# Kernel tuning notes

Hardware: AMD Instinct MI355X
Metric: run time of the kernel (lower is better)

The kernel has to match this reference:

```python
import jax, jax.numpy as jnp
import numpy as np

VOCAB = 100000
DIM = 300
N, P, D = 4096, 10, 17  # samples, paths per sample (2C), padded path depth


def setup_inputs() -> dict:
    key = jax.random.key(0)
    k1, k2, k3, k4, k5 = jax.random.split(key, 5)
    word_idx = jax.random.randint(k1, (N,), 0, VOCAB)
    paths = jax.random.randint(k2, (N, P, D), 0, VOCAB - 1)   # inner-node ids
    labels = jax.random.randint(k3, (N, P, D), 0, 2)          # branch directions
    emb1 = jax.random.normal(k4, (VOCAB, DIM), dtype=jnp.float32) * 0.1
    emb2 = jax.random.normal(k5, (VOCAB - 1, DIM), dtype=jnp.float32) * 0.1
    return {"word_idx": word_idx, "paths": paths, "labels": labels,
            "emb1": emb1, "emb2": emb2}


def reference(word_idx, paths, labels, emb1, emb2):
    # proj = embedding_1(x_idx): [N, DIM]
    proj = emb1[word_idx]
    # hierarchy_vectors = embedding_2(dir_path): [N, P, D, DIM]
    hvecs = emb2[paths]
    # output = sigmoid(proj @ hvecs.T), batched over (N, P): [N, P, D]
    logits = jnp.einsum('nd,npkd->npk', proj, hvecs)
    output = jax.nn.sigmoid(logits)
    # mask[output >= 0.5] = 1; target[mask == label] = 1
    mask = (output >= 0.5).astype(labels.dtype)
    target = (mask == labels).astype(jnp.float32)
    return output, target
```

## Files before the change

kernel.cpp:

```cpp
#include <hip/hip_runtime.h>
#include <math.h>

#define NN 4096
#define PP 10
#define DD 17
#define DIM 300
#define NPD (NN * PP * DD)

__global__ __launch_bounds__(256) void hs_fwd_kernel(
    const int* __restrict__ word_idx,
    const int* __restrict__ paths,
    const int* __restrict__ labels,
    const float* __restrict__ emb1,
    const float* __restrict__ emb2,
    float* __restrict__ out,
    float* __restrict__ target)
{
    const int wave = (int)((blockIdx.x * blockDim.x + threadIdx.x) >> 6);
    const int lane = (int)(threadIdx.x & 63);
    if (wave >= NN * PP) return;
    const int n = wave / PP;

    const float* e1 = emb1 + (long long)word_idx[n] * DIM;
    const float pr0 = e1[lane];
    const float pr1 = e1[lane + 64];
    const float pr2 = e1[lane + 128];
    const float pr3 = e1[lane + 192];
    const float pr4 = (lane < DIM - 256) ? e1[lane + 256] : 0.0f;

    const long long base = (long long)wave * DD;
    const int my_path  = (lane < DD) ? paths[base + lane]  : 0;
    const int my_label = (lane < DD) ? labels[base + lane] : 0;

    float my_logit = 0.0f;
    #pragma unroll
    for (int k = 0; k < DD; ++k) {
        const int row = __shfl(my_path, k);
        const float* e2 = emb2 + (long long)row * DIM;
        float acc = pr0 * e2[lane]
                  + pr1 * e2[lane + 64]
                  + pr2 * e2[lane + 128]
                  + pr3 * e2[lane + 192];
        if (lane < DIM - 256) acc += pr4 * e2[lane + 256];
        #pragma unroll
        for (int off = 32; off > 0; off >>= 1)
            acc += __shfl_xor(acc, off);
        if (lane == k) my_logit = acc;
    }

    if (lane < DD) {
        const float o = 1.0f / (1.0f + expf(-my_logit));
        out[base + lane] = o;
        const int mask = (o >= 0.5f) ? 1 : 0;
        target[base + lane] = (mask == my_label) ? 1.0f : 0.0f;
    }
}

extern "C" void kernel_launch(void* const* d_in, const int* in_sizes, int n_in,
                              void* d_out, int out_size, void* d_ws, size_t ws_size,
                              hipStream_t stream) {
    const int*   word_idx = (const int*)d_in[0];
    const int*   paths    = (const int*)d_in[1];
    const int*   labels   = (const int*)d_in[2];
    const float* emb1     = (const float*)d_in[3];
    const float* emb2     = (const float*)d_in[4];

    float* out    = (float*)d_out;
    float* target = (float*)d_out + NPD;

    const int total_waves = NN * PP;
    const int waves_per_block = 4;
    const int blocks = (total_waves + waves_per_block - 1) / waves_per_block;

    hs_fwd_kernel<<<blocks, 256, 0, stream>>>(word_idx, paths, labels, emb1, emb2, out, target);
}
```

Baseline: 324.1 us.

## Vectorize embedding loads as float4 and process two path rows per wave

Embedding rows are now read as float4, and each wave splits into two 32-lane halves, each handling a different path node at once. This cuts the number of load instructions and the loop iterations (9 instead of 17) and shortens each shuffle reduction to 5 steps plus one cross-half exchange. The float4 loads require each 300-float row to be 16-byte aligned, which holds since 300*4 is a multiple of 16. The unused half in the last iteration does wasted shuffles.

```diff
diff --git a/kernel.cpp b/kernel.cpp
--- a/kernel.cpp
+++ b/kernel.cpp
@@ -20,32 +20,42 @@
     const int lane = (int)(threadIdx.x & 63);
     if (wave >= NN * PP) return;
     const int n = wave / PP;
+    const int j    = lane & 31;
+    const int half = lane >> 5;
 
-    const float* e1 = emb1 + (long long)word_idx[n] * DIM;
-    const float pr0 = e1[lane];
-    const float pr1 = e1[lane + 64];
-    const float pr2 = e1[lane + 128];
-    const float pr3 = e1[lane + 192];
-    const float pr4 = (lane < DIM - 256) ? e1[lane + 256] : 0.0f;
+    const float4* p4 = (const float4*)(emb1 + (long long)word_idx[n] * DIM);
+    const float4 pr0 = p4[j];
+    const float4 pr1 = p4[j + 32];
+    const float4 pr2 = (j < 11) ? p4[j + 64] : make_float4(0.f, 0.f, 0.f, 0.f);
 
     const long long base = (long long)wave * DD;
     const int my_path  = (lane < DD) ? paths[base + lane]  : 0;
     const int my_label = (lane < DD) ? labels[base + lane] : 0;
 
     float my_logit = 0.0f;
+
     #pragma unroll
-    for (int k = 0; k < DD; ++k) {
-        const int row = __shfl(my_path, k);
-        const float* e2 = emb2 + (long long)row * DIM;
-        float acc = pr0 * e2[lane]
-                  + pr1 * e2[lane + 64]
-                  + pr2 * e2[lane + 128]
-                  + pr3 * e2[lane + 192];
-        if (lane < DIM - 256) acc += pr4 * e2[lane + 256];
+    for (int i = 0; i < 9; ++i) {
+        const int k = 2 * i + half;
+        float acc = 0.0f;
+        if (k < DD) {
+            const int row = __shfl(my_path, k);
+            const float4* r4 = (const float4*)(emb2 + (long long)row * DIM);
+            const float4 a0 = r4[j];
+            const float4 a1 = r4[j + 32];
+            acc = pr0.x * a0.x + pr0.y * a0.y + pr0.z * a0.z + pr0.w * a0.w
+                + pr1.x * a1.x + pr1.y * a1.y + pr1.z * a1.z + pr1.w * a1.w;
+            if (j < 11) {
+                const float4 a2 = r4[j + 64];
+                acc += pr2.x * a2.x + pr2.y * a2.y + pr2.z * a2.z + pr2.w * a2.w;
+            }
+        }
         #pragma unroll
-        for (int off = 32; off > 0; off >>= 1)
+        for (int off = 16; off > 0; off >>= 1)
             acc += __shfl_xor(acc, off);
-        if (lane == k) my_logit = acc;
+        const float other = __shfl_xor(acc, 32);
+        if (lane == 2 * i) my_logit = acc;
+        if (2 * i + 1 < DD && lane == 2 * i + 1) my_logit = other;
     }
 
     if (lane < DD) {
```

Result: no change. 322.9 us (-0.4%).

## Bucket path entries by emb2 row block and compute from LDS-staged rows

Applied to the files above, without the earlier changes.

Replaces the per-(sample,path) wave gather with a counting sort: it builds a histogram of path entries over 32-row buckets of emb2, scans it, and scatters (row, entry) records. A compute kernel then loads each 32-row emb2 tile into LDS once and processes every entry that hits it, gathering only the emb1 row per entry and software-prefetching the next entry. This turns random emb2 row reads into one streaming read of the table, at the cost of extra kernel launches, atomics, and scattered writes of out/target. Falls back to the old kernel if the workspace is too small.

```diff
diff --git a/kernel.cpp b/kernel.cpp
--- a/kernel.cpp
+++ b/kernel.cpp
@@ -6,48 +6,179 @@
 #define DD 17
 #define DIM 300
 #define NPD (NN * PP * DD)
-
-__global__ __launch_bounds__(256) void hs_fwd_kernel(
+#define NENT NPD
+#define NROWS 99999
+#define RPB 32
+#define NB ((NROWS + RPB - 1) / RPB)
+#define NBPAD 3136
+#define BPL 49
+
+
+__global__ void zero_kernel(unsigned* cnt) {
+    for (int i = threadIdx.x; i < NBPAD; i += 256) cnt[i] = 0;
+}
+
+__global__ void hist_kernel(const int* __restrict__ paths, unsigned* __restrict__ cnt) {
+    const int e = blockIdx.x * 256 + threadIdx.x;
+    const unsigned b = ((unsigned)paths[e]) >> 5;
+    atomicAdd(&cnt[b], 1u);
+}
+
+__global__ void scan_kernel(const unsigned* __restrict__ cnt,
+                            unsigned* __restrict__ off, unsigned* __restrict__ cur) {
+    const int lane = threadIdx.x;
+    unsigned local[BPL];
+    unsigned s = 0;
+    const int base = lane * BPL;
+    #pragma unroll
+    for (int j = 0; j < BPL; ++j) { local[j] = s; s += cnt[base + j]; }
+    unsigned t = s;
+    #pragma unroll
+    for (int o = 1; o < 64; o <<= 1) {
+        unsigned u = __shfl_up(t, o);
+        if (lane >= o) t += u;
+    }
+    const unsigned excl = t - s;
+    #pragma unroll
+    for (int j = 0; j < BPL; ++j) {
+        const unsigned v = excl + local[j];
+        off[base + j] = v;
+        cur[base + j] = v;
+    }
+}
+
+__global__ void scatter_kernel(const int* __restrict__ paths,
+                               unsigned* __restrict__ cur,
+                               unsigned long long* __restrict__ rec) {
+    const int e = blockIdx.x * 256 + threadIdx.x;
+    const int row = paths[e];
+    const unsigned b = ((unsigned)row) >> 5;
+    const unsigned pos = atomicAdd(&cur[b], 1u);
+    rec[pos] = (((unsigned long long)(unsigned)row) << 32) | (unsigned)e;
+}
+
+
+struct Ent { int e; int rl; bool v; float4 a0, a1, a2; };
+
+__device__ __forceinline__ void load_entry(
+    int t, unsigned start, unsigned end, int wv, int h, int j, long long r0,
+    const unsigned long long* __restrict__ rec,
     const int* __restrict__ word_idx,
-    const int* __restrict__ paths,
+    const float* __restrict__ emb1, Ent& E)
+{
+    const int i = (int)start + 2 * (wv + t * 4) + h;
+    E.v = i < (int)end;
+    const int ic = E.v ? i : (int)start;
+    const unsigned long long r = rec[ic];
+    E.e = (int)(r & 0xffffffffULL);
+    const int row = (int)(r >> 32);
+    E.rl = row - (int)r0;
+    const int n = E.e / 170;
+    const int wr = word_idx[n];
+    const float4* pp = (const float4*)(emb1 + (long long)wr * DIM);
+    E.a0 = pp[j];
+    E.a1 = pp[j + 32];
+    E.a2 = (j < 11) ? pp[j + 64] : make_float4(0.f, 0.f, 0.f, 0.f);
+}
+
+__global__ __launch_bounds__(256, 4) void compute_kernel(
+    const int* __restrict__ word_idx,
     const int* __restrict__ labels,
     const float* __restrict__ emb1,
     const float* __restrict__ emb2,
-    float* __restrict__ out,
-    float* __restrict__ target)
+    const unsigned* __restrict__ off,
+    const unsigned long long* __restrict__ rec,
+    float* __restrict__ out, float* __restrict__ target)
+{
+    __shared__ float lds[RPB * DIM];
+    const int b = blockIdx.x;
+    const int tid = threadIdx.x;
+    const long long r0 = (long long)b * RPB;
+    const int nr = (NROWS - r0 < RPB) ? (int)(NROWS - r0) : RPB;
+
+    {
+        const float4* src4 = (const float4*)(emb2 + r0 * DIM);
+        float4* l4 = (float4*)lds;
+        const int nf4 = nr * (DIM / 4);
+        for (int t = tid; t < nf4; t += 256) l4[t] = src4[t];
+    }
+    __syncthreads();
+
+    const int lane = tid & 63;
+    const int wv = tid >> 6;
+    const int h = lane >> 5;
+    const int j = lane & 31;
+
+    const unsigned start = off[b];
+    const unsigned end = off[b + 1];
+    const int cnt = (int)(end - start);
+    const int mywork = cnt - 2 * wv;
+    const int niter = (mywork > 0) ? ((mywork + 7) >> 3) : 0;
+    if (niter == 0) return;
+
+    Ent C;
+    load_entry(0, start, end, wv, h, j, r0, rec, word_idx, emb1, C);
+
+    for (int t = 0; t < niter; ++t) {
+        Ent Nx;
+        if (t + 1 < niter)
+            load_entry(t + 1, start, end, wv, h, j, r0, rec, word_idx, emb1, Nx);
+
+        const float4* r4 = (const float4*)(lds + C.rl * DIM);
+        const float4 c0 = r4[j];
+        const float4 c1 = r4[j + 32];
+        float acc = C.a0.x * c0.x + C.a0.y * c0.y + C.a0.z * c0.z + C.a0.w * c0.w
+                  + C.a1.x * c1.x + C.a1.y * c1.y + C.a1.z * c1.z + C.a1.w * c1.w;
+        if (j < 11) {
+            const float4 c2 = r4[j + 64];
+            acc += C.a2.x * c2.x + C.a2.y * c2.y + C.a2.z * c2.z + C.a2.w * c2.w;
+        }
+        #pragma unroll
+        for (int o = 16; o > 0; o >>= 1)
+            acc += __shfl_xor(acc, o);
+
+        if (C.v && j == 0) {
+            const float o_ = 1.0f / (1.0f + expf(-acc));
+            out[C.e] = o_;
+            const int m = (o_ >= 0.5f) ? 1 : 0;
+            const int lb = labels[C.e];
+            target[C.e] = (m == lb) ? 1.0f : 0.0f;
+        }
+        if (t + 1 < niter) C = Nx;
+    }
+}
+
+
+__global__ __launch_bounds__(256) void hs_fwd_fallback(
+    const int* __restrict__ word_idx, const int* __restrict__ paths,
+    const int* __restrict__ labels, const float* __restrict__ emb1,
+    const float* __restrict__ emb2, float* __restrict__ out, float* __restrict__ target)
 {
     const int wave = (int)((blockIdx.x * blockDim.x + threadIdx.x) >> 6);
     const int lane = (int)(threadIdx.x & 63);
     if (wave >= NN * PP) return;
     const int n = wave / PP;
-
     const float* e1 = emb1 + (long long)word_idx[n] * DIM;
     const float pr0 = e1[lane];
     const float pr1 = e1[lane + 64];
     const float pr2 = e1[lane + 128];
     const float pr3 = e1[lane + 192];
     const float pr4 = (lane < DIM - 256) ? e1[lane + 256] : 0.0f;
-
     const long long base = (long long)wave * DD;
     const int my_path  = (lane < DD) ? paths[base + lane]  : 0;
     const int my_label = (lane < DD) ? labels[base + lane] : 0;
-
     float my_logit = 0.0f;
     #pragma unroll
     for (int k = 0; k < DD; ++k) {
         const int row = __shfl(my_path, k);
         const float* e2 = emb2 + (long long)row * DIM;
-        float acc = pr0 * e2[lane]
-                  + pr1 * e2[lane + 64]
-                  + pr2 * e2[lane + 128]
+        float acc = pr0 * e2[lane] + pr1 * e2[lane + 64] + pr2 * e2[lane + 128]
                   + pr3 * e2[lane + 192];
         if (lane < DIM - 256) acc += pr4 * e2[lane + 256];
         #pragma unroll
-        for (int off = 32; off > 0; off >>= 1)
-            acc += __shfl_xor(acc, off);
+        for (int o = 32; o > 0; o >>= 1) acc += __shfl_xor(acc, o);
         if (lane == k) my_logit = acc;
     }
-
     if (lane < DD) {
         const float o = 1.0f / (1.0f + expf(-my_logit));
         out[base + lane] = o;
@@ -55,6 +186,7 @@
         target[base + lane] = (mask == my_label) ? 1.0f : 0.0f;
     }
 }
+
 
 extern "C" void kernel_launch(void* const* d_in, const int* in_sizes, int n_in,
                               void* d_out, int out_size, void* d_ws, size_t ws_size,
@@ -68,9 +200,23 @@
     float* out    = (float*)d_out;
     float* target = (float*)d_out + NPD;
 
-    const int total_waves = NN * PP;
-    const int waves_per_block = 4;
-    const int blocks = (total_waves + waves_per_block - 1) / waves_per_block;
-
-    hs_fwd_kernel<<<blocks, 256, 0, stream>>>(word_idx, paths, labels, emb1, emb2, out, target);
-}
+    const size_t rec_off = (size_t)NBPAD * 3 * sizeof(unsigned);
+    const size_t need = rec_off + (size_t)NENT * sizeof(unsigned long long);
+
+    if (ws_size < need) {
+        const int blocks = (NN * PP + 3) / 4;
+        hs_fwd_fallback<<<blocks, 256, 0, stream>>>(word_idx, paths, labels, emb1, emb2, out, target);
+        return;
+    }
+
+    unsigned* cnt = (unsigned*)d_ws;
+    unsigned* off = cnt + NBPAD;
+    unsigned* cur = off + NBPAD;
+    unsigned long long* rec = (unsigned long long*)((char*)d_ws + rec_off);
+
+    zero_kernel<<<1, 256, 0, stream>>>(cnt);
+    hist_kernel<<<NENT / 256, 256, 0, stream>>>(paths, cnt);
+    scan_kernel<<<1, 64, 0, stream>>>(cnt, off, cur);
+    scatter_kernel<<<NENT / 256, 256, 0, stream>>>(paths, cur, rec);
+    compute_kernel<<<NB, 256, 0, stream>>>(word_idx, labels, emb1, emb2, off, rec, out, target);
+}
```

Result: slower. 522.7 us (+61.3%).

## Gather from per-call fp16 copy of emb2, with fp32 refinement of near-threshold logits

Applied to the files above, without the earlier changes.

Each call first converts the whole emb2 table to fp16 in workspace. The main kernel then gathers half-width rows with vectorized uint2 and float4 loads, which is meant to halve the bytes moved by the random row gathers. Logits whose magnitude falls below a small threshold are appended to a list through an atomic counter, and a refine kernel recomputes just those entries in fp32 so the thresholded target stays correct. The trade is a full-table read and write on every call, plus an extra launch and small fp16 rounding errors in the sigmoid outputs.

```diff
diff --git a/kernel.cpp b/kernel.cpp
--- a/kernel.cpp
+++ b/kernel.cpp
@@ -1,4 +1,5 @@
 #include <hip/hip_runtime.h>
+#include <hip/hip_fp16.h>
 #include <math.h>
 
 #define NN 4096
@@ -6,27 +7,46 @@
 #define DD 17
 #define DIM 300
 #define NPD (NN * PP * DD)
+#define NROWS 99999
+#define TAB_HALFS (29999700LL)
+#define TAB_F4 (7499925LL)
+#define DELTA 0.004f
 
-__global__ __launch_bounds__(256) void hs_fwd_kernel(
-    const int* __restrict__ word_idx,
-    const int* __restrict__ paths,
-    const int* __restrict__ labels,
-    const float* __restrict__ emb1,
-    const float* __restrict__ emb2,
-    float* __restrict__ out,
-    float* __restrict__ target)
+#define TAB_OFF 2785344ULL
+#define WS_NEED (TAB_OFF + TAB_HALFS * 2ULL)
+
+__global__ __launch_bounds__(256) void convert_kernel(
+    const float* __restrict__ src, ushort* __restrict__ dst, unsigned* __restrict__ counter)
+{
+    if (blockIdx.x == 0 && threadIdx.x == 0) *counter = 0;
+    const long long stride = (long long)gridDim.x * blockDim.x;
+    const float4* s4 = (const float4*)src;
+    uint2* d2 = (uint2*)dst;
+    for (long long i = blockIdx.x * (long long)blockDim.x + threadIdx.x; i < TAB_F4; i += stride) {
+        const float4 f = s4[i];
+        const __half2 h0 = __floats2half2_rn(f.x, f.y);
+        const __half2 h1 = __floats2half2_rn(f.z, f.w);
+        uint2 u;
+        u.x = *(const unsigned*)&h0;
+        u.y = *(const unsigned*)&h1;
+        d2[i] = u;
+    }
+}
+
+__global__ __launch_bounds__(256) void main_fp16(
+    const int* __restrict__ word_idx, const int* __restrict__ paths,
+    const int* __restrict__ labels, const float* __restrict__ emb1,
+    const ushort* __restrict__ tab, float* __restrict__ out, float* __restrict__ target,
+    unsigned* __restrict__ counter, unsigned* __restrict__ list)
 {
     const int wave = (int)((blockIdx.x * blockDim.x + threadIdx.x) >> 6);
     const int lane = (int)(threadIdx.x & 63);
     if (wave >= NN * PP) return;
     const int n = wave / PP;
 
-    const float* e1 = emb1 + (long long)word_idx[n] * DIM;
-    const float pr0 = e1[lane];
-    const float pr1 = e1[lane + 64];
-    const float pr2 = e1[lane + 128];
-    const float pr3 = e1[lane + 192];
-    const float pr4 = (lane < DIM - 256) ? e1[lane + 256] : 0.0f;
+    const float4* p4 = (const float4*)(emb1 + (long long)word_idx[n] * DIM);
+    const float4 p0 = p4[lane];
+    const float4 p1 = (lane < 11) ? p4[lane + 64] : make_float4(0.f, 0.f, 0.f, 0.f);
 
     const long long base = (long long)wave * DD;
     const int my_path  = (lane < DD) ? paths[base + lane]  : 0;
@@ -36,18 +56,95 @@
     #pragma unroll
     for (int k = 0; k < DD; ++k) {
         const int row = __shfl(my_path, k);
-        const float* e2 = emb2 + (long long)row * DIM;
-        float acc = pr0 * e2[lane]
-                  + pr1 * e2[lane + 64]
-                  + pr2 * e2[lane + 128]
-                  + pr3 * e2[lane + 192];
-        if (lane < DIM - 256) acc += pr4 * e2[lane + 256];
+        const uint2* q2 = (const uint2*)(tab + (long long)row * DIM);
+        const uint2 a = q2[lane];
+        const float2 f0 = __half22float2(*(const __half2*)&a.x);
+        const float2 f1 = __half22float2(*(const __half2*)&a.y);
+        float acc = p0.x * f0.x + p0.y * f0.y + p0.z * f1.x + p0.w * f1.y;
+        if (lane < 11) {
+            const uint2 b = q2[lane + 64];
+            const float2 g0 = __half22float2(*(const __half2*)&b.x);
+            const float2 g1 = __half22float2(*(const __half2*)&b.y);
+            acc += p1.x * g0.x + p1.y * g0.y + p1.z * g1.x + p1.w * g1.y;
+        }
         #pragma unroll
         for (int off = 32; off > 0; off >>= 1)
             acc += __shfl_xor(acc, off);
         if (lane == k) my_logit = acc;
     }
 
+    if (lane < DD) {
+        const float o = 1.0f / (1.0f + expf(-my_logit));
+        out[base + lane] = o;
+        const int mask = (o >= 0.5f) ? 1 : 0;
+        target[base + lane] = (mask == my_label) ? 1.0f : 0.0f;
+        if (fabsf(my_logit) < DELTA) {
+            const unsigned idx = atomicAdd(counter, 1u);
+            list[idx] = (unsigned)(base + lane);
+        }
+    }
+}
+
+__global__ __launch_bounds__(256) void refine_kernel(
+    const int* __restrict__ word_idx, const int* __restrict__ paths,
+    const int* __restrict__ labels, const float* __restrict__ emb1,
+    const float* __restrict__ emb2, const unsigned* __restrict__ counter,
+    const unsigned* __restrict__ list, float* __restrict__ out, float* __restrict__ target)
+{
+    const int wid  = (int)((blockIdx.x * blockDim.x + threadIdx.x) >> 6);
+    const int lane = (int)(threadIdx.x & 63);
+    const int nflag = (int)*counter;
+    const int nw = (int)(gridDim.x * (blockDim.x >> 6));
+    for (int idx = wid; idx < nflag; idx += nw) {
+        const int e = (int)list[idx];
+        const int n = e / (PP * DD);
+        const float* p = emb1 + (long long)word_idx[n] * DIM;
+        const float* h = emb2 + (long long)paths[e] * DIM;
+        float acc = p[lane] * h[lane] + p[lane + 64] * h[lane + 64]
+                  + p[lane + 128] * h[lane + 128] + p[lane + 192] * h[lane + 192];
+        if (lane < DIM - 256) acc += p[lane + 256] * h[lane + 256];
+        #pragma unroll
+        for (int off = 32; off > 0; off >>= 1)
+            acc += __shfl_xor(acc, off);
+        if (lane == 0) {
+            const float o = 1.0f / (1.0f + expf(-acc));
+            out[e] = o;
+            const int mask = (o >= 0.5f) ? 1 : 0;
+            target[e] = (mask == labels[e]) ? 1.0f : 0.0f;
+        }
+    }
+}
+
+__global__ __launch_bounds__(256) void hs_fwd_fallback(
+    const int* __restrict__ word_idx, const int* __restrict__ paths,
+    const int* __restrict__ labels, const float* __restrict__ emb1,
+    const float* __restrict__ emb2, float* __restrict__ out, float* __restrict__ target)
+{
+    const int wave = (int)((blockIdx.x * blockDim.x + threadIdx.x) >> 6);
+    const int lane = (int)(threadIdx.x & 63);
+    if (wave >= NN * PP) return;
+    const int n = wave / PP;
+    const float* e1 = emb1 + (long long)word_idx[n] * DIM;
+    const float pr0 = e1[lane];
+    const float pr1 = e1[lane + 64];
+    const float pr2 = e1[lane + 128];
+    const float pr3 = e1[lane + 192];
+    const float pr4 = (lane < DIM - 256) ? e1[lane + 256] : 0.0f;
+    const long long base = (long long)wave * DD;
+    const int my_path  = (lane < DD) ? paths[base + lane]  : 0;
+    const int my_label = (lane < DD) ? labels[base + lane] : 0;
+    float my_logit = 0.0f;
+    #pragma unroll
+    for (int k = 0; k < DD; ++k) {
+        const int row = __shfl(my_path, k);
+        const float* e2 = emb2 + (long long)row * DIM;
+        float acc = pr0 * e2[lane] + pr1 * e2[lane + 64] + pr2 * e2[lane + 128]
+                  + pr3 * e2[lane + 192];
+        if (lane < DIM - 256) acc += pr4 * e2[lane + 256];
+        #pragma unroll
+        for (int o = 32; o > 0; o >>= 1) acc += __shfl_xor(acc, o);
+        if (lane == k) my_logit = acc;
+    }
     if (lane < DD) {
         const float o = 1.0f / (1.0f + expf(-my_logit));
         out[base + lane] = o;
@@ -68,9 +165,19 @@
     float* out    = (float*)d_out;
     float* target = (float*)d_out + NPD;
 
-    const int total_waves = NN * PP;
-    const int waves_per_block = 4;
-    const int blocks = (total_waves + waves_per_block - 1) / waves_per_block;
+    if (ws_size < WS_NEED) {
+        const int blocks = (NN * PP + 3) / 4;
+        hs_fwd_fallback<<<blocks, 256, 0, stream>>>(word_idx, paths, labels, emb1, emb2, out, target);
+        return;
+    }
 
-    hs_fwd_kernel<<<blocks, 256, 0, stream>>>(word_idx, paths, labels, emb1, emb2, out, target);
+    unsigned* counter = (unsigned*)d_ws;
+    unsigned* list    = counter + 2;
+    ushort*   tab     = (ushort*)((char*)d_ws + TAB_OFF);
+
+    convert_kernel<<<4096, 256, 0, stream>>>(emb2, tab, counter);
+    main_fp16<<<(NN * PP + 3) / 4, 256, 0, stream>>>(word_idx, paths, labels, emb1, tab,
+                                                     out, target, counter, list);
+    refine_kernel<<<256, 256, 0, stream>>>(word_idx, paths, labels, emb1, emb2,
+                                           counter, list, out, target);
 }
```

Result: slower. 423.0 us (+30.5%).
